# Optimization experiments

Hardware: AMD Instinct MI355X
Metric: run time of the kernel (lower is better)

## Reference

```python
import jax, jax.numpy as jnp
import numpy as np

N_NODES = 1000
ALPHA = 0.1  # LeakyReLU negative slope


def gcn_conv(x, edge_index, W, b):
    """PyG GCNConv: add self-loops, symmetric deg^{-1/2} normalization,
    linear transform, scatter-add aggregation at destination, plus bias."""
    n = x.shape[0]
    src, dst = edge_index[0], edge_index[1]
    loop = jnp.arange(n, dtype=src.dtype)
    src = jnp.concatenate([src, loop])
    dst = jnp.concatenate([dst, loop])
    deg = jax.ops.segment_sum(jnp.ones(src.shape[0], dtype=x.dtype), dst, num_segments=n)
    dinv = jnp.where(deg > 0, jax.lax.rsqrt(jnp.maximum(deg, 1e-12)), 0.0)
    norm = dinv[src] * dinv[dst]                     # [E+n]
    h = x @ W                                        # [n, out]
    out = jax.ops.segment_sum(norm[:, None] * h[src], dst, num_segments=n)
    return out + b


def leaky_relu(x):
    return jnp.where(x > 0, x, ALPHA * x)


def setup_inputs() -> dict:
    key = jax.random.key(0)
    ks = jax.random.split(key, 16)
    F_in, D, H = 128, 512, 256
    x = jax.random.normal(ks[0], (N_NODES, F_in), dtype=jnp.float32)
    edge_index = jax.random.randint(ks[1], (2, 64000), 0, N_NODES, dtype=jnp.int64)

    def lin(k, fan_in, fan_out):
        s = 1.0 / np.sqrt(fan_in)
        kw, kb = jax.random.split(k)
        W = jax.random.uniform(kw, (fan_in, fan_out), minval=-s, maxval=s, dtype=jnp.float32)
        b = jax.random.uniform(kb, (fan_out,), minval=-s, maxval=s, dtype=jnp.float32)
        return W, b

    W1, b1 = lin(ks[2], F_in, D)
    W2, b2 = lin(ks[3], D, D)
    W3, b3 = lin(ks[4], D, D)
    Wd1, bd1 = lin(ks[5], N_NODES * D, H)
    Wd2, bd2 = lin(ks[6], H, H)
    Wd3, bd3 = lin(ks[7], H, H)
    Wd4, bd4 = lin(ks[8], H, 1)
    return {"x": x, "edge_index": edge_index,
            "W1": W1, "b1": b1, "W2": W2, "b2": b2, "W3": W3, "b3": b3,
            "Wd1": Wd1, "bd1": bd1, "Wd2": Wd2, "bd2": bd2,
            "Wd3": Wd3, "bd3": bd3, "Wd4": Wd4, "bd4": bd4}


def reference(x, edge_index, W1, b1, W2, b2, W3, b3,
              Wd1, bd1, Wd2, bd2, Wd3, bd3, Wd4, bd4):
    h = jnp.tanh(gcn_conv(x, edge_index, W1, b1))
    h = jnp.tanh(gcn_conv(h, edge_index, W2, b2))
    h = jnp.tanh(gcn_conv(h, edge_index, W3, b3))
    f = h.reshape(-1)                                # flatten [N*D]
    f = leaky_relu(f @ Wd1 + bd1)
    f = leaky_relu(f @ Wd2 + bd2)
    f = leaky_relu(f @ Wd3 + bd3)
    out = f @ Wd4 + bd4                              # [1]
    return out
```

## Files before the change

### kernel.cpp

```cpp
#include <hip/hip_runtime.h>
#include <math.h>

#define N_NODES 1000
#define E_EDGES 64000
#define STRIDE  256

typedef float fx4 __attribute__((ext_vector_type(4)));
typedef float fx2 __attribute__((ext_vector_type(2)));

__device__ inline float lrelu(float v){ return v > 0.f ? v : 0.1f * v; }

__global__ __launch_bounds__(512)
void k0(const int* __restrict__ src, const int* __restrict__ dst,
        int* __restrict__ cnt, int* __restrict__ csr){
  int e = blockIdx.x * 512 + threadIdx.x;
  int s = src[e], d = dst[e];
  int pos = atomicAdd(&cnt[d], 1);
  if (pos < STRIDE) csr[(d << 8) + pos] = s;
}

__global__ __launch_bounds__(1024)
void kA(const float* __restrict__ x, const int* __restrict__ cnt,
        const int* __restrict__ csr, const float* __restrict__ W1,
        const float* __restrict__ b1, const float* __restrict__ W2,
        float* __restrict__ hs2){
  __shared__ float dinv_lds[1024];
  __shared__ fx4 gsum[4][8][32];
  __shared__ float xa[4 * 128];
  __shared__ float h1s[4 * 512];
  __shared__ fx4 red[7][4][128];
  int b = blockIdx.x, t = threadIdx.x;
  dinv_lds[t] = (t < N_NODES) ? rsqrtf((float)(cnt[t] + 1)) : 0.f;
  __syncthreads();
  {
    int q = t >> 8, tt = t & 255;
    int c = tt & 31, sl = tt >> 5;
    int n = b * 4 + q;
    int m = cnt[n]; if (m > STRIDE) m = STRIDE;
    const fx4* x4 = (const fx4*)x;
    const int* row = csr + (n << 8);
    fx4 acc = {0.f, 0.f, 0.f, 0.f};
    if (sl == 0) acc = dinv_lds[n] * x4[n * 32 + c];
    for (int i = sl; i < m; i += 8){
      int sv = row[i];
      acc += dinv_lds[sv] * x4[sv * 32 + c];
    }
    gsum[q][sl][c] = acc;
    __syncthreads();
    if (sl < 4) gsum[q][sl][c] += gsum[q][sl + 4][c];
    __syncthreads();
    if (sl < 2) gsum[q][sl][c] += gsum[q][sl + 2][c];
    __syncthreads();
    if (sl == 0)
      ((fx4*)xa)[q * 32 + c] = dinv_lds[n] * (gsum[q][0][c] + gsum[q][1][c]);
    __syncthreads();
  }
  int cq = t & 127, kh = t >> 7;
  {
    fx4 a0 = {0,0,0,0}, a1 = {0,0,0,0}, a2 = {0,0,0,0}, a3 = {0,0,0,0};
    int kb = kh * 16;
    const fx4* Wp = (const fx4*)W1 + (size_t)kb * 128 + cq;
    #pragma unroll
    for (int k = 0; k < 16; ++k){
      fx4 w = Wp[k * 128];
      float h0 = xa[0 * 128 + kb + k], h1 = xa[1 * 128 + kb + k];
      float h2 = xa[2 * 128 + kb + k], h3 = xa[3 * 128 + kb + k];
      a0 += h0 * w; a1 += h1 * w; a2 += h2 * w; a3 += h3 * w;
    }
    if (kh > 0){
      red[kh-1][0][cq] = a0; red[kh-1][1][cq] = a1;
      red[kh-1][2][cq] = a2; red[kh-1][3][cq] = a3;
    }
    __syncthreads();
    if (kh == 0){
      #pragma unroll
      for (int s = 0; s < 7; ++s){
        a0 += red[s][0][cq]; a1 += red[s][1][cq];
        a2 += red[s][2][cq]; a3 += red[s][3][cq];
      }
      fx4 bb = ((const fx4*)b1)[cq];
      fx4* H = (fx4*)h1s;
      fx4 o;
      o.x=tanhf(a0.x+bb.x); o.y=tanhf(a0.y+bb.y); o.z=tanhf(a0.z+bb.z); o.w=tanhf(a0.w+bb.w); H[0*128+cq]=o;
      o.x=tanhf(a1.x+bb.x); o.y=tanhf(a1.y+bb.y); o.z=tanhf(a1.z+bb.z); o.w=tanhf(a1.w+bb.w); H[1*128+cq]=o;
      o.x=tanhf(a2.x+bb.x); o.y=tanhf(a2.y+bb.y); o.z=tanhf(a2.z+bb.z); o.w=tanhf(a2.w+bb.w); H[2*128+cq]=o;
      o.x=tanhf(a3.x+bb.x); o.y=tanhf(a3.y+bb.y); o.z=tanhf(a3.z+bb.z); o.w=tanhf(a3.w+bb.w); H[3*128+cq]=o;
    }
    __syncthreads();
  }
  {
    fx4 a0 = {0,0,0,0}, a1 = {0,0,0,0}, a2 = {0,0,0,0}, a3 = {0,0,0,0};
    int kb = kh * 64;
    const fx4* Wp = (const fx4*)W2 + (size_t)kb * 128 + cq;
    #pragma unroll 8
    for (int k = 0; k < 64; ++k){
      fx4 w = Wp[k * 128];
      float h0 = h1s[0 * 512 + kb + k], h1 = h1s[1 * 512 + kb + k];
      float h2 = h1s[2 * 512 + kb + k], h3 = h1s[3 * 512 + kb + k];
      a0 += h0 * w; a1 += h1 * w; a2 += h2 * w; a3 += h3 * w;
    }
    if (kh > 0){
      red[kh-1][0][cq] = a0; red[kh-1][1][cq] = a1;
      red[kh-1][2][cq] = a2; red[kh-1][3][cq] = a3;
    }
    __syncthreads();
    if (kh == 0){
      #pragma unroll
      for (int s = 0; s < 7; ++s){
        a0 += red[s][0][cq]; a1 += red[s][1][cq];
        a2 += red[s][2][cq]; a3 += red[s][3][cq];
      }
      int r0 = b * 4;
      fx4* O = (fx4*)hs2;
      O[(size_t)(r0 + 0) * 128 + cq] = a0 * dinv_lds[r0 + 0];
      O[(size_t)(r0 + 1) * 128 + cq] = a1 * dinv_lds[r0 + 1];
      O[(size_t)(r0 + 2) * 128 + cq] = a2 * dinv_lds[r0 + 2];
      O[(size_t)(r0 + 3) * 128 + cq] = a3 * dinv_lds[r0 + 3];
    }
  }
}

__global__ __launch_bounds__(1024)
void kB(const float* __restrict__ hs_in, const int* __restrict__ cnt,
        const int* __restrict__ csr, const float* __restrict__ bias,
        const float* __restrict__ W, float* __restrict__ hs_out){
  __shared__ float h2l[4 * 512];
  __shared__ fx4 hpart[4][128];
  __shared__ fx4 red[7][4][128];
  int b = blockIdx.x, t = threadIdx.x;
  {
    int q = t >> 8, tt = t & 255;
    int c = tt & 127, half = tt >> 7;
    int n = b * 4 + q;
    int m = cnt[n]; if (m > STRIDE) m = STRIDE;
    const fx4* h4 = (const fx4*)hs_in;
    const int* row = csr + (n << 8);
    fx4 s = {0.f, 0.f, 0.f, 0.f};
    if (half == 0) s = h4[n * 128 + c];
    int i = half;
    for (; i + 6 < m; i += 8){
      int s0 = row[i], s1 = row[i + 2], s2 = row[i + 4], s3 = row[i + 6];
      s += h4[s0 * 128 + c] + h4[s1 * 128 + c]
         + h4[s2 * 128 + c] + h4[s3 * 128 + c];
    }
    for (; i < m; i += 2) s += h4[row[i] * 128 + c];
    if (half == 1) hpart[q][c] = s;
    __syncthreads();
    if (half == 0){
      s += hpart[q][c];
      float dn = rsqrtf((float)(m + 1));
      fx4 bb = ((const fx4*)bias)[c];
      fx4 o;
      o.x = tanhf(dn * s.x + bb.x);
      o.y = tanhf(dn * s.y + bb.y);
      o.z = tanhf(dn * s.z + bb.z);
      o.w = tanhf(dn * s.w + bb.w);
      ((fx4*)h2l)[q * 128 + c] = o;
    }
    __syncthreads();
  }
  int cq = t & 127, kh = t >> 7;
  fx4 a0 = {0,0,0,0}, a1 = {0,0,0,0}, a2 = {0,0,0,0}, a3 = {0,0,0,0};
  int kb = kh * 64;
  const fx4* Wp = (const fx4*)W + (size_t)kb * 128 + cq;
  #pragma unroll 8
  for (int k = 0; k < 64; ++k){
    fx4 w = Wp[k * 128];
    float h0 = h2l[0 * 512 + kb + k], h1 = h2l[1 * 512 + kb + k];
    float h2 = h2l[2 * 512 + kb + k], h3 = h2l[3 * 512 + kb + k];
    a0 += h0 * w; a1 += h1 * w; a2 += h2 * w; a3 += h3 * w;
  }
  if (kh > 0){
    red[kh-1][0][cq] = a0; red[kh-1][1][cq] = a1;
    red[kh-1][2][cq] = a2; red[kh-1][3][cq] = a3;
  }
  __syncthreads();
  if (kh == 0){
    #pragma unroll
    for (int s = 0; s < 7; ++s){
      a0 += red[s][0][cq]; a1 += red[s][1][cq];
      a2 += red[s][2][cq]; a3 += red[s][3][cq];
    }
    int r0 = b * 4;
    fx4* O = (fx4*)hs_out;
    O[(size_t)(r0 + 0) * 128 + cq] = a0 * rsqrtf((float)(cnt[r0 + 0] + 1));
    O[(size_t)(r0 + 1) * 128 + cq] = a1 * rsqrtf((float)(cnt[r0 + 1] + 1));
    O[(size_t)(r0 + 2) * 128 + cq] = a2 * rsqrtf((float)(cnt[r0 + 2] + 1));
    O[(size_t)(r0 + 3) * 128 + cq] = a3 * rsqrtf((float)(cnt[r0 + 3] + 1));
  }
}

__global__ __launch_bounds__(1024)
void kC(const float* __restrict__ hs_in, const int* __restrict__ cnt,
        const int* __restrict__ csr, const float* __restrict__ bias,
        const float* __restrict__ Wd1, float* __restrict__ partial,
        int* __restrict__ done,
        const float* __restrict__ bd1,
        const float* __restrict__ Wd2, const float* __restrict__ bd2,
        const float* __restrict__ Wd3, const float* __restrict__ bd3,
        const float* __restrict__ Wd4, const float* __restrict__ bd4,
        float* __restrict__ out){
  __shared__ float f_lds[2048];
  __shared__ fx4 red4[1024];
  __shared__ float y[256];
  __shared__ int flag;
  int b = blockIdx.x, t = threadIdx.x;
  if (b < 8){
    const fx4* w2 = (const fx4*)Wd2;
    const fx4* w3 = (const fx4*)Wd3;
    fx4 v0 = w2[b * 2048 + t] + w3[b * 2048 + t];
    fx4 v1 = w2[b * 2048 + 1024 + t] + w3[b * 2048 + 1024 + t];
    float dm = v0.x + v1.x;
    asm volatile("" :: "v"(dm));
  }
  int q = t >> 8, tt = t & 255;
  int n = b * 4 + q;
  int m = cnt[n]; if (m > STRIDE) m = STRIDE;
  float dn = rsqrtf((float)(m + 1));
  const fx2* h2 = (const fx2*)hs_in;
  const int* row = csr + (n << 8);
  fx2 s = h2[n * 256 + tt];
  int i = 0;
  for (; i + 4 <= m; i += 4){
    int4 s4 = *(const int4*)(row + i);
    s += h2[s4.x * 256 + tt] + h2[s4.y * 256 + tt]
       + h2[s4.z * 256 + tt] + h2[s4.w * 256 + tt];
  }
  for (; i < m; ++i) s += h2[row[i] * 256 + tt];
  fx2 bb = ((const fx2*)bias)[tt];
  fx2 o;
  o.x = tanhf(dn * s.x + bb.x);
  o.y = tanhf(dn * s.y + bb.y);
  ((fx2*)f_lds)[q * 256 + tt] = o;
  __syncthreads();
  int r = t >> 6, c = t & 63;
  const fx4* W4 = (const fx4*)Wd1 + (size_t)b * 131072 + c;
  fx4 acc = {0.f, 0.f, 0.f, 0.f};
  #pragma unroll 8
  for (int it = 0; it < 128; ++it){
    int i2 = it * 16 + r;
    acc += f_lds[i2] * __builtin_nontemporal_load(&W4[(size_t)i2 * 64]);
  }
  red4[t] = acc;
  __syncthreads();
  if (t < 512) red4[t] += red4[t + 512];
  __syncthreads();
  if (t < 256) red4[t] += red4[t + 256];
  __syncthreads();
  if (t < 128) red4[t] += red4[t + 128];
  __syncthreads();
  if (t < 64) ((fx4*)(partial + b * 256))[t] = red4[t] + red4[t + 64];
  __syncthreads();
  if (t == 0){
    __threadfence();
    int old = atomicAdd(done, 1);
    flag = (old == 249);
  }
  __syncthreads();
  if (!flag) return;
  __threadfence();
  float* sm = (float*)red4;
  int c2 = t & 255, h = t >> 8;
  float sum = 0.f;
  for (int bb2 = h; bb2 < 250; bb2 += 4) sum += partial[bb2 * 256 + c2];
  sm[t] = sum;
  __syncthreads();
  if (t < 512) sm[t] += sm[t + 512];
  __syncthreads();
  if (t < 256) y[t] = lrelu(sm[t] + sm[t + 256] + bd1[t]);
  __syncthreads();
  float a = 0.f;
  #pragma unroll 4
  for (int i3 = h * 64; i3 < h * 64 + 64; ++i3) a += y[i3] * Wd2[i3 * 256 + c2];
  sm[t] = a;
  __syncthreads();
  if (t < 512) sm[t] += sm[t + 512];
  __syncthreads();
  if (t < 256) y[t] = lrelu(sm[t] + sm[t + 256] + bd2[t]);
  __syncthreads();
  a = 0.f;
  #pragma unroll 4
  for (int i3 = h * 64; i3 < h * 64 + 64; ++i3) a += y[i3] * Wd3[i3 * 256 + c2];
  sm[t] = a;
  __syncthreads();
  if (t < 512) sm[t] += sm[t + 512];
  __syncthreads();
  if (t < 256) y[t] = lrelu(sm[t] + sm[t + 256] + bd3[t]);
  __syncthreads();
  sm[t] = (t < 256) ? y[t] * Wd4[t] : 0.f;
  __syncthreads();
  for (int off = 128; off > 0; off >>= 1){
    if (t < off) sm[t] += sm[t + off];
    __syncthreads();
  }
  if (t == 0) out[0] = sm[0] + bd4[0];
}


extern "C" void kernel_launch(void* const* d_in, const int* in_sizes, int n_in,
                              void* d_out, int out_size, void* d_ws, size_t ws_size,
                              hipStream_t stream) {
  const float* x   = (const float*)d_in[0];
  const int*   ei  = (const int*)  d_in[1];
  const float* W1  = (const float*)d_in[2];  const float* b1  = (const float*)d_in[3];
  const float* W2  = (const float*)d_in[4];  const float* b2  = (const float*)d_in[5];
  const float* W3  = (const float*)d_in[6];  const float* b3  = (const float*)d_in[7];
  const float* Wd1 = (const float*)d_in[8];  const float* bd1 = (const float*)d_in[9];
  const float* Wd2 = (const float*)d_in[10]; const float* bd2 = (const float*)d_in[11];
  const float* Wd3 = (const float*)d_in[12]; const float* bd3 = (const float*)d_in[13];
  const float* Wd4 = (const float*)d_in[14]; const float* bd4 = (const float*)d_in[15];
  float* out = (float*)d_out;

  const int* src = ei;
  const int* dst = ei + E_EDGES;

  char* ws = (char*)d_ws;
  int*   cnt     = (int*)  (ws + 0);
  int*   done    = (int*)  (ws + 4096);
  int*   csr     = (int*)  (ws + 8192);
  float* hsA     = (float*)(ws + 1114112);
  float* hsB     = (float*)(ws + 1114112 + 2097152);
  float* partial = (float*)(ws + 1114112 + 2 * 2097152);

  (void)hipMemsetAsync(ws, 0, 8192, stream);
  k0<<<125, 512, 0, stream>>>(src, dst, cnt, csr);
  kA<<<250, 1024, 0, stream>>>(x, cnt, csr, W1, b1, W2, hsA);
  kB<<<250, 1024, 0, stream>>>(hsA, cnt, csr, b2, W3, hsB);
  kC<<<250, 1024, 0, stream>>>(hsB, cnt, csr, b3, Wd1, partial, done,
                               bd1, Wd2, bd2, Wd3, bd3, Wd4, bd4, out);
}
```

Baseline: 200.3 us.

## Fuse CSR build into first GCN kernel and prefetch Wd1 in dense stage

The separate CSR-building kernel is folded into kA: the first 125 blocks do the edge scatter, then every block spin-waits on a global counter before computing degrees. This removes one kernel launch but assumes all 250 blocks are co-resident, otherwise the spin-wait deadlocks. In kC, the first 8 iterations of Wd1 loads are issued before the neighbour aggregation so they overlap it. The aggregation is reorganised to use fx4 loads split across two half-groups with an LDS reduction.

```diff
diff --git a/kernel.cpp b/kernel.cpp
--- a/kernel.cpp
+++ b/kernel.cpp
@@ -6,30 +6,37 @@
 #define STRIDE  256
 
 typedef float fx4 __attribute__((ext_vector_type(4)));
-typedef float fx2 __attribute__((ext_vector_type(2)));
 
 __device__ inline float lrelu(float v){ return v > 0.f ? v : 0.1f * v; }
 
-__global__ __launch_bounds__(512)
-void k0(const int* __restrict__ src, const int* __restrict__ dst,
-        int* __restrict__ cnt, int* __restrict__ csr){
-  int e = blockIdx.x * 512 + threadIdx.x;
-  int s = src[e], d = dst[e];
-  int pos = atomicAdd(&cnt[d], 1);
-  if (pos < STRIDE) csr[(d << 8) + pos] = s;
-}
-
 __global__ __launch_bounds__(1024)
-void kA(const float* __restrict__ x, const int* __restrict__ cnt,
-        const int* __restrict__ csr, const float* __restrict__ W1,
-        const float* __restrict__ b1, const float* __restrict__ W2,
-        float* __restrict__ hs2){
+void kA(const int* __restrict__ src, const int* __restrict__ dst,
+        const float* __restrict__ x, int* __restrict__ cnt,
+        int* __restrict__ csr, int* __restrict__ built,
+        const float* __restrict__ W1, const float* __restrict__ b1,
+        const float* __restrict__ W2, float* __restrict__ hs2){
   __shared__ float dinv_lds[1024];
   __shared__ fx4 gsum[4][8][32];
   __shared__ float xa[4 * 128];
   __shared__ float h1s[4 * 512];
   __shared__ fx4 red[7][4][128];
   int b = blockIdx.x, t = threadIdx.x;
+  if (b < 125){
+    if (t < 512){
+      int e = b * 512 + t;
+      int s = src[e], d = dst[e];
+      int pos = atomicAdd(&cnt[d], 1);
+      if (pos < STRIDE) csr[(d << 8) + pos] = s;
+    }
+    __syncthreads();
+    if (t == 0)
+      __hip_atomic_fetch_add(built, 1, __ATOMIC_RELEASE, __HIP_MEMORY_SCOPE_AGENT);
+  }
+  if (t == 0){
+    while (__hip_atomic_load(built, __ATOMIC_ACQUIRE, __HIP_MEMORY_SCOPE_AGENT) < 125)
+      __builtin_amdgcn_s_sleep(16);
+  }
+  __syncthreads();
   dinv_lds[t] = (t < N_NODES) ? rsqrtf((float)(cnt[t] + 1)) : 0.f;
   __syncthreads();
   {
@@ -205,6 +212,12 @@
   __shared__ float y[256];
   __shared__ int flag;
   int b = blockIdx.x, t = threadIdx.x;
+  int r = t >> 6, c = t & 63;
+  const fx4* W4 = (const fx4*)Wd1 + (size_t)b * 131072 + c;
+  fx4 w_pre[8];
+  #pragma unroll
+  for (int j = 0; j < 8; ++j)
+    w_pre[j] = __builtin_nontemporal_load(&W4[(size_t)(j * 16 + r) * 64]);
   if (b < 8){
     const fx4* w2 = (const fx4*)Wd2;
     const fx4* w3 = (const fx4*)Wd3;
@@ -213,31 +226,43 @@
     float dm = v0.x + v1.x;
     asm volatile("" :: "v"(dm));
   }
-  int q = t >> 8, tt = t & 255;
-  int n = b * 4 + q;
-  int m = cnt[n]; if (m > STRIDE) m = STRIDE;
-  float dn = rsqrtf((float)(m + 1));
-  const fx2* h2 = (const fx2*)hs_in;
-  const int* row = csr + (n << 8);
-  fx2 s = h2[n * 256 + tt];
-  int i = 0;
-  for (; i + 4 <= m; i += 4){
-    int4 s4 = *(const int4*)(row + i);
-    s += h2[s4.x * 256 + tt] + h2[s4.y * 256 + tt]
-       + h2[s4.z * 256 + tt] + h2[s4.w * 256 + tt];
-  }
-  for (; i < m; ++i) s += h2[row[i] * 256 + tt];
-  fx2 bb = ((const fx2*)bias)[tt];
-  fx2 o;
-  o.x = tanhf(dn * s.x + bb.x);
-  o.y = tanhf(dn * s.y + bb.y);
-  ((fx2*)f_lds)[q * 256 + tt] = o;
-  __syncthreads();
-  int r = t >> 6, c = t & 63;
-  const fx4* W4 = (const fx4*)Wd1 + (size_t)b * 131072 + c;
+  {
+    int q = t >> 8, tt = t & 255;
+    int cc = tt & 127, half = tt >> 7;
+    int n = b * 4 + q;
+    int m = cnt[n]; if (m > STRIDE) m = STRIDE;
+    const fx4* h4 = (const fx4*)hs_in;
+    const int* row = csr + (n << 8);
+    fx4 s = {0.f, 0.f, 0.f, 0.f};
+    if (half == 0) s = h4[n * 128 + cc];
+    int i = half;
+    for (; i + 6 < m; i += 8){
+      int s0 = row[i], s1 = row[i + 2], s2 = row[i + 4], s3 = row[i + 6];
+      s += h4[s0 * 128 + cc] + h4[s1 * 128 + cc]
+         + h4[s2 * 128 + cc] + h4[s3 * 128 + cc];
+    }
+    for (; i < m; i += 2) s += h4[row[i] * 128 + cc];
+    if (half == 1) ((fx4*)red4)[q * 128 + cc] = s;
+    __syncthreads();
+    if (half == 0){
+      s += ((fx4*)red4)[q * 128 + cc];
+      float dn = rsqrtf((float)(m + 1));
+      fx4 bb = ((const fx4*)bias)[cc];
+      fx4 o;
+      o.x = tanhf(dn * s.x + bb.x);
+      o.y = tanhf(dn * s.y + bb.y);
+      o.z = tanhf(dn * s.z + bb.z);
+      o.w = tanhf(dn * s.w + bb.w);
+      ((fx4*)f_lds)[q * 128 + cc] = o;
+    }
+    __syncthreads();
+  }
   fx4 acc = {0.f, 0.f, 0.f, 0.f};
+  #pragma unroll
+  for (int j = 0; j < 8; ++j)
+    acc += f_lds[j * 16 + r] * w_pre[j];
   #pragma unroll 8
-  for (int it = 0; it < 128; ++it){
+  for (int it = 8; it < 128; ++it){
     int i2 = it * 16 + r;
     acc += f_lds[i2] * __builtin_nontemporal_load(&W4[(size_t)i2 * 64]);
   }
@@ -317,14 +342,14 @@
   char* ws = (char*)d_ws;
   int*   cnt     = (int*)  (ws + 0);
   int*   done    = (int*)  (ws + 4096);
+  int*   built   = (int*)  (ws + 4160);
   int*   csr     = (int*)  (ws + 8192);
   float* hsA     = (float*)(ws + 1114112);
   float* hsB     = (float*)(ws + 1114112 + 2097152);
   float* partial = (float*)(ws + 1114112 + 2 * 2097152);
 
   (void)hipMemsetAsync(ws, 0, 8192, stream);
-  k0<<<125, 512, 0, stream>>>(src, dst, cnt, csr);
-  kA<<<250, 1024, 0, stream>>>(x, cnt, csr, W1, b1, W2, hsA);
+  kA<<<250, 1024, 0, stream>>>(src, dst, x, cnt, csr, built, W1, b1, W2, hsA);
   kB<<<250, 1024, 0, stream>>>(hsA, cnt, csr, b2, W3, hsB);
   kC<<<250, 1024, 0, stream>>>(hsB, cnt, csr, b3, Wd1, partial, done,
                                bd1, Wd2, bd2, Wd3, bd3, Wd4, bd4, out);
```

Result: slower. 221.2 us (+10.4%).
